# Performance work log

Measured on AMD Instinct MI355X. Metric: run time of the kernel, lower is better.

## Reference

```python
import jax, jax.numpy as jnp
import numpy as np

FORGET_BIAS = 1.0  # tf.nn.rnn_cell.LSTMCell default


def _lstm_scan(x_btE, W, b, hidden):
    """x: (B,T,E). W: (E+H, 4H), gate order i, j, f, o (TF LSTMCell)."""
    B = x_btE.shape[0]
    h0 = jnp.zeros((B, hidden), x_btE.dtype)
    c0 = jnp.zeros((B, hidden), x_btE.dtype)

    def step(carry, x_t):
        h, c = carry
        z = jnp.concatenate([x_t, h], axis=-1) @ W + b  # (B, 4H)
        i, j, f, o = jnp.split(z, 4, axis=-1)
        c_new = jax.nn.sigmoid(f + FORGET_BIAS) * c + jax.nn.sigmoid(i) * jnp.tanh(j)
        h_new = jax.nn.sigmoid(o) * jnp.tanh(c_new)
        return (h_new, c_new), h_new

    (_, _), hs = jax.lax.scan(step, (h0, c0), jnp.swapaxes(x_btE, 0, 1))
    return jnp.swapaxes(hs, 0, 1)  # (B, T, H)


def setup_inputs() -> dict:
    key = jax.random.key(0)
    ks = jax.random.split(key, 5)
    B, T, V, E, H, C = 256, 120, 50000, 256, 1024, 5
    tokens = jax.random.randint(ks[0], (B, T, 1), 0, V, dtype=jnp.int32)
    embeddings = jax.random.normal(ks[1], (V, E), jnp.float32) * 0.1
    W_lstm = jax.random.normal(ks[2], (E + H, 4 * H), jnp.float32) * (1.0 / np.sqrt(E + H))
    b_lstm = jnp.zeros((4 * H,), jnp.float32)
    U = jax.random.normal(ks[3], (H, C), jnp.float32) * (1.0 / np.sqrt(H))
    b2 = jnp.zeros((C,), jnp.float32)
    return {"tokens": tokens, "embeddings": embeddings, "W_lstm": W_lstm,
            "b_lstm": b_lstm, "U": U, "b2": b2}


def reference(tokens, embeddings, W_lstm, b_lstm, U, b2):
    B, T, F = tokens.shape  # F == n_features == 1
    E = embeddings.shape[1]
    H = U.shape[0]
    # embedding lookup + reshape to (B, T, F*E)
    x = embeddings[tokens].reshape(B, T, F * E)
    outputs = _lstm_scan(x, W_lstm, b_lstm, H)  # (B, T, H); dropout keep_prob=1 -> identity
    preds = outputs.reshape(-1, H) @ U + b2
    return preds.reshape(B, T, -1)  # (B, max_length, n_classes)
```

## Files before the change

kernel.cpp:

```cpp
#include <hip/hip_runtime.h>

typedef unsigned short u16;
typedef unsigned int u32;
typedef unsigned long long u64;
typedef int   v4i  __attribute__((ext_vector_type(4)));
typedef short v8s  __attribute__((ext_vector_type(8)));
typedef float v2f  __attribute__((ext_vector_type(2)));
typedef float v16f __attribute__((ext_vector_type(16)));

#define B_ 256
#define T_ 120
#define E_ 256
#define H_ 1024
#define K_ 1280
#define LDH 1032
#define LDX 264

#define WS_WF   0
#define WS_X    10485760
#define WS_HS   26214400
#define WS_BAR  89128960

__device__ __forceinline__ u16 f2bf(float f) {
    union { float f; u32 u; } v; v.f = f;
    u32 r = v.u + 0x7fffu + ((v.u >> 16) & 1u);
    return (u16)(r >> 16);
}
__device__ __forceinline__ float bf2f(u16 u) {
    union { u32 u; float f; } v; v.u = ((u32)u) << 16; return v.f;
}
__device__ __forceinline__ float fsig(float x) {
    float t = __builtin_amdgcn_exp2f(-1.44269504f * x);
    return __builtin_amdgcn_rcpf(1.0f + t);
}
__device__ __forceinline__ float ftanh_(float x) {
    float xc = fminf(8.0f, fmaxf(-8.0f, x));
    float t = __builtin_amdgcn_exp2f(2.88539008f * xc);
    return (t - 1.0f) * __builtin_amdgcn_rcpf(t + 1.0f);
}
__device__ __forceinline__ void gl_lds16(const void* g, void* l) {
    __builtin_amdgcn_global_load_lds(
        (const __attribute__((address_space(1))) void*)g,
        (__attribute__((address_space(3))) void*)l, 16, 0, 0);
}

__global__ void prep_fused(const float* __restrict__ W, u16* __restrict__ Wf,
                           const int* __restrict__ tokens, const float* __restrict__ emb,
                           u16* __restrict__ X, u32* __restrict__ bar) {
    __shared__ u16 tile[32 * 136];
    int bx  = blockIdx.x;
    int tid = threadIdx.x;

    if (bx < 1280) {
        if (bx == 0) {
            v4i z = {0, 0, 0, 0};
            *(v4i*)(bar + tid * 4) = z;
        }
        int cid = bx / 5, fo = bx % 5;
        int kh  = cid & 1, g = (cid >> 1) & 3, nc = cid >> 3;
        int colbase = g * 1024 + nc * 32;
        int c = tid & 31, r = tid >> 5;

#pragma unroll
        for (int fl = 0; fl < 8; ++fl) {
            int k0 = (2 * (fo * 8 + fl) + kh) * 16;
#pragma unroll
            for (int rr = 0; rr < 2; ++rr) {
                int row = r + rr * 8;
                float v = W[(size_t)(k0 + row) * 4096 + colbase + c];
                tile[c * 136 + fl * 16 + row] = f2bf(v);
            }
        }
        __syncthreads();

        int lane = tid & 63;
#pragma unroll
        for (int pass = 0; pass < 2; ++pass) {
            int fl = (tid >> 6) + pass * 4;
            v4i o = *(const v4i*)&tile[(lane & 31) * 136 + fl * 16 + ((lane >> 5) << 3)];
            *(v4i*)(Wf + (((size_t)(cid * 40 + fo * 8 + fl)) << 9) + lane * 8) = o;
        }
    } else {
        int v   = (bx - 1280) * 256 + tid;
        int e8  = v & 31;
        int row = v >> 5;
        int t = row >> 8, b = row & 255;
        int tok = tokens[b * T_ + t];
        const float* src = emb + (size_t)tok * E_ + e8 * 8;
        u16 o[8];
#pragma unroll
        for (int j = 0; j < 8; ++j) o[j] = f2bf(src[j]);
        *(v4i*)(X + (size_t)row * E_ + e8 * 8) = *(v4i*)o;
    }
}

__global__ __launch_bounds__(512, 2) void lstm_main(
    const u16* __restrict__ Wf, const u16* __restrict__ X,
    const float* __restrict__ b_lstm, u16* __restrict__ hs,
    u32* __restrict__ bar) {

    __shared__ u16  hbuf[32 * LDH];
    __shared__ u16  xbuf[32 * LDX];
    __shared__ float gates[2 * 4 * 32 * 34];
    __shared__ float bias[128];

    const int tid   = threadIdx.x;
    const int lane  = tid & 63;
    const int wv    = tid >> 6;
    const int g     = wv >> 1;
    const int khalf = wv & 1;
    const int bid   = blockIdx.x;
    const int mchunk = bid & 7;
    const int nc    = bid >> 3;
    const int m0    = mchunk << 5;

    if (tid < 128) bias[tid] = b_lstm[(tid >> 5) * H_ + (nc << 5) + (tid & 31)];

    v8s Wr[40];
    {
        const int cid = nc * 8 + g * 2 + khalf;
        const v4i* wsrc = (const v4i*)(Wf + (size_t)cid * 40 * 512);
#pragma unroll
        for (int f = 0; f < 40; ++f)
            Wr[f] = __builtin_bit_cast(v8s, wsrc[f * 64 + lane]);
    }
#pragma unroll
    for (int f = 0; f < 40; ++f) asm volatile("" : "+v"(Wr[f]));

    {
        const v4i* xs = (const v4i*)(X + (size_t)m0 * E_);
#pragma unroll
        for (int i = 0; i < 2; ++i) {
            int idx = tid + i * 512;
            int r = idx >> 5, c8 = idx & 31;
            *(v4i*)&xbuf[r * LDX + c8 * 8] = xs[r * 32 + c8];
        }
    }
    __syncthreads();

    const u16* Ax = &xbuf[(lane & 31) * LDX + ((lane >> 5) << 3)];
    const u16* Ah = &hbuf[(lane & 31) * LDH + ((lane >> 5) << 3)];

    v16f acc = {0,0,0,0,0,0,0,0,0,0,0,0,0,0,0,0};
#pragma unroll
    for (int f = 0; f < 8; ++f) {
        v8s a = *(const v8s*)(Ax + (2 * f + khalf) * 16);
        acc = __builtin_amdgcn_mfma_f32_32x32x16_bf16(a, Wr[f], acc, 0, 0, 0);
    }

    float cst[2] = {0.f, 0.f};
    const int cm  = tid >> 4;
    const int cn2 = (tid & 15) << 1;
    u32* hs32 = (u32*)hs;

    for (int t = 0; t < T_; ++t) {
        if (t > 0) {
            if (wv == 0) {
                u32* p = &bar[(mchunk * 32 + (lane & 31)) * 4];
                for (;;) {
                    u32 v = __hip_atomic_load(p, __ATOMIC_RELAXED,
                                              __HIP_MEMORY_SCOPE_AGENT);
                    if (__all(v >= (u32)t)) break;
                    __builtin_amdgcn_s_sleep(1);
                }
            }
            __syncthreads();
            {
                const u16* srcb = hs + ((size_t)(t - 1) * B_ + m0) * H_;
                int r0 = wv << 2;
#pragma unroll
                for (int half = 0; half < 2; ++half)
#pragma unroll
                    for (int i = 0; i < 4; ++i) {
                        int r = r0 + i;
                        gl_lds16(srcb + (size_t)r * H_ + half * 512 + lane * 8,
                                 &hbuf[r * LDH + half * 512]);
                    }
            }
            asm volatile("s_waitcnt vmcnt(4)\n\ts_barrier" ::: "memory");
#pragma unroll
            for (int f = 8; f < 24; ++f) {
                v8s a = *(const v8s*)(Ah + ((2 * f + khalf) * 16 - 256));
                acc = __builtin_amdgcn_mfma_f32_32x32x16_bf16(a, Wr[f], acc, 0, 0, 0);
            }
            asm volatile("s_waitcnt vmcnt(0)\n\ts_barrier" ::: "memory");
#pragma unroll
            for (int f = 24; f < 40; ++f) {
                v8s a = *(const v8s*)(Ah + ((2 * f + khalf) * 16 - 256));
                acc = __builtin_amdgcn_mfma_f32_32x32x16_bf16(a, Wr[f], acc, 0, 0, 0);
            }
        }

        {
            float* gb = &gates[((khalf << 2) + g) * 1088];
            int col = lane & 31, rq = (lane >> 5) << 2;
#pragma unroll
            for (int reg = 0; reg < 16; ++reg) {
                int row = (reg & 3) + ((reg >> 2) << 3) + rq;
                gb[row * 34 + col] = acc[reg];
            }
        }
        __syncthreads();

        if (t + 1 < T_) {
            const v4i* xs = (const v4i*)(X + ((size_t)(t + 1) * B_ + m0) * E_);
#pragma unroll
            for (int i = 0; i < 2; ++i) {
                int idx = tid + i * 512;
                int r = idx >> 5, c8 = idx & 31;
                *(v4i*)&xbuf[r * LDX + c8 * 8] = xs[r * 32 + c8];
            }
        }

        u32 hpack = 0;
        {
            v2f zz[4];
#pragma unroll
            for (int gg = 0; gg < 4; ++gg) {
                v2f a = *(const v2f*)&gates[gg * 1088 + cm * 34 + cn2];
                v2f b = *(const v2f*)&gates[(4 + gg) * 1088 + cm * 34 + cn2];
                zz[gg].x = a.x + b.x; zz[gg].y = a.y + b.y;
            }
#pragma unroll
            for (int q = 0; q < 2; ++q) {
                int n = cn2 + q;
                float ip = zz[0][q] + bias[n];
                float jp = zz[1][q] + bias[32 + n];
                float fp = zz[2][q] + bias[64 + n] + 1.0f;
                float op = zz[3][q] + bias[96 + n];
                float cc = fsig(fp) * cst[q] + fsig(ip) * ftanh_(jp);
                cst[q] = cc;
                hpack |= ((u32)f2bf(fsig(op) * ftanh_(cc))) << (16 * q);
            }
        }
        __hip_atomic_store(&hs32[((size_t)t * B_ + m0 + cm) * 512 + (nc << 4) + (tid & 15)],
                           hpack, __ATOMIC_RELAXED, __HIP_MEMORY_SCOPE_AGENT);

        if (t + 1 < T_) {
            asm volatile("s_waitcnt vmcnt(0)" ::: "memory");
            __syncthreads();
            if (tid == 0)
                __hip_atomic_store(&bar[(mchunk * 32 + nc) * 4], (u32)(t + 1),
                                   __ATOMIC_RELAXED, __HIP_MEMORY_SCOPE_AGENT);
#pragma unroll
            for (int reg = 0; reg < 16; ++reg) acc[reg] = 0.f;
#pragma unroll
            for (int f = 0; f < 8; ++f) {
                v8s a = *(const v8s*)(Ax + (2 * f + khalf) * 16);
                acc = __builtin_amdgcn_mfma_f32_32x32x16_bf16(a, Wr[f], acc, 0, 0, 0);
            }
        }
    }
}

__global__ void proj_kernel(const u16* __restrict__ hs, const float* __restrict__ U,
                            const float* __restrict__ b2, float* __restrict__ out) {
    __shared__ float Ul[H_ * 5];
    int tid = threadIdx.x;
    for (int i = tid; i < H_ * 5; i += 256) Ul[i] = U[i];
    __syncthreads();
    int wv = tid >> 6, lane = tid & 63;
#pragma unroll 1
    for (int i = 0; i < 16; ++i) {
        int row = blockIdx.x * 64 + wv * 16 + i;
        int t = row >> 8, b = row & 255;
        const v4i* hp = (const v4i*)(hs + (size_t)row * H_);
        float p[5] = {0.f, 0.f, 0.f, 0.f, 0.f};
#pragma unroll
        for (int half = 0; half < 2; ++half) {
            v4i hv = hp[lane * 2 + half];
            u16 us[8];
            *(v4i*)us = hv;
#pragma unroll
            for (int j = 0; j < 8; ++j) {
                float hf = bf2f(us[j]);
                int k = lane * 16 + half * 8 + j;
#pragma unroll
                for (int c = 0; c < 5; ++c) p[c] += hf * Ul[k * 5 + c];
            }
        }
#pragma unroll
        for (int c = 0; c < 5; ++c)
            for (int off = 32; off > 0; off >>= 1)
                p[c] += __shfl_down(p[c], off, 64);
        if (lane == 0) {
#pragma unroll
            for (int c = 0; c < 5; ++c)
                out[((size_t)b * T_ + t) * 5 + c] = p[c] + b2[c];
        }
    }
}

extern "C" void kernel_launch(void* const* d_in, const int* in_sizes, int n_in,
                              void* d_out, int out_size, void* d_ws, size_t ws_size,
                              hipStream_t stream) {
    const int*   tokens = (const int*)d_in[0];
    const float* emb    = (const float*)d_in[1];
    const float* W      = (const float*)d_in[2];
    const float* b_l    = (const float*)d_in[3];
    const float* U      = (const float*)d_in[4];
    const float* b2     = (const float*)d_in[5];
    float* out = (float*)d_out;

    char* ws = (char*)d_ws;
    u16* Wf  = (u16*)(ws + WS_WF);
    u16* X   = (u16*)(ws + WS_X);
    u16* hs  = (u16*)(ws + WS_HS);
    u32* bar = (u32*)(ws + WS_BAR);

    prep_fused<<<5120, 256, 0, stream>>>(W, Wf, tokens, emb, X, bar);
    lstm_main<<<256, 512, 0, stream>>>(Wf, X, b_l, hs, bar);
    proj_kernel<<<480, 256, 0, stream>>>(hs, U, b2, out);
}
```

Before: 581.0 us.

## Split LSTM gate GEMM into K-quarters per wave with two gate accumulators

Each wave now computes two gates over one quarter of the K dimension instead of one gate over half of K. Each LDS A-fragment read is reused for two MFMAs, which halves the LDS A traffic and gives two independent accumulator chains. The cost is more gate partial sums to store in LDS and reduce (four per gate), plus an extra accumulator's registers. The next-step x tile is also prefetched into registers at the top of the step so the global load overlaps the barrier wait.

```diff
diff --git a/kernel.cpp b/kernel.cpp
--- a/kernel.cpp
+++ b/kernel.cpp
@@ -101,14 +101,14 @@
 
     __shared__ u16  hbuf[32 * LDH];
     __shared__ u16  xbuf[32 * LDX];
-    __shared__ float gates[2 * 4 * 32 * 34];
+    __shared__ float gates[16 * 32 * 34];
     __shared__ float bias[128];
 
     const int tid   = threadIdx.x;
     const int lane  = tid & 63;
     const int wv    = tid >> 6;
-    const int g     = wv >> 1;
-    const int khalf = wv & 1;
+    const int kq    = wv & 3;
+    const int gg    = wv >> 2;
     const int bid   = blockIdx.x;
     const int mchunk = bid & 7;
     const int nc    = bid >> 3;
@@ -117,12 +117,16 @@
     if (tid < 128) bias[tid] = b_lstm[(tid >> 5) * H_ + (nc << 5) + (tid & 31)];
 
     v8s Wr[40];
-    {
-        const int cid = nc * 8 + g * 2 + khalf;
-        const v4i* wsrc = (const v4i*)(Wf + (size_t)cid * 40 * 512);
-#pragma unroll
-        for (int f = 0; f < 40; ++f)
-            Wr[f] = __builtin_bit_cast(v8s, wsrc[f * 64 + lane]);
+#pragma unroll
+    for (int j = 0; j < 20; ++j) {
+#pragma unroll
+        for (int gb = 0; gb < 2; ++gb) {
+            int s    = 4 * j + kq;
+            int gate = gg * 2 + gb;
+            int cid  = nc * 8 + gate * 2 + (s & 1);
+            const v4i* wsrc = (const v4i*)(Wf + (((size_t)(cid * 40 + (s >> 1))) << 9));
+            Wr[j * 2 + gb] = __builtin_bit_cast(v8s, wsrc[lane]);
+        }
     }
 #pragma unroll
     for (int f = 0; f < 40; ++f) asm volatile("" : "+v"(Wr[f]));
@@ -132,8 +136,7 @@
 #pragma unroll
         for (int i = 0; i < 2; ++i) {
             int idx = tid + i * 512;
-            int r = idx >> 5, c8 = idx & 31;
-            *(v4i*)&xbuf[r * LDX + c8 * 8] = xs[r * 32 + c8];
+            *(v4i*)&xbuf[(idx >> 5) * LDX + (idx & 31) * 8] = xs[idx];
         }
     }
     __syncthreads();
@@ -141,11 +144,13 @@
     const u16* Ax = &xbuf[(lane & 31) * LDX + ((lane >> 5) << 3)];
     const u16* Ah = &hbuf[(lane & 31) * LDH + ((lane >> 5) << 3)];
 
-    v16f acc = {0,0,0,0,0,0,0,0,0,0,0,0,0,0,0,0};
-#pragma unroll
-    for (int f = 0; f < 8; ++f) {
-        v8s a = *(const v8s*)(Ax + (2 * f + khalf) * 16);
-        acc = __builtin_amdgcn_mfma_f32_32x32x16_bf16(a, Wr[f], acc, 0, 0, 0);
+    v16f accA = {0,0,0,0,0,0,0,0,0,0,0,0,0,0,0,0};
+    v16f accB = {0,0,0,0,0,0,0,0,0,0,0,0,0,0,0,0};
+#pragma unroll
+    for (int j = 0; j < 4; ++j) {
+        v8s a = *(const v8s*)(Ax + (4 * j + kq) * 16);
+        accA = __builtin_amdgcn_mfma_f32_32x32x16_bf16(a, Wr[2 * j],     accA, 0, 0, 0);
+        accB = __builtin_amdgcn_mfma_f32_32x32x16_bf16(a, Wr[2 * j + 1], accB, 0, 0, 0);
     }
 
     float cst[2] = {0.f, 0.f};
@@ -154,6 +159,13 @@
     u32* hs32 = (u32*)hs;
 
     for (int t = 0; t < T_; ++t) {
+        v4i xr0, xr1;
+        if (t + 1 < T_) {
+            const v4i* xs = (const v4i*)(X + ((size_t)(t + 1) * B_ + m0) * E_);
+            xr0 = xs[tid];
+            xr1 = xs[tid + 512];
+        }
+
         if (t > 0) {
             if (wv == 0) {
                 u32* p = &bar[(mchunk * 32 + (lane & 31)) * 4];
@@ -179,47 +191,51 @@
             }
             asm volatile("s_waitcnt vmcnt(4)\n\ts_barrier" ::: "memory");
 #pragma unroll
-            for (int f = 8; f < 24; ++f) {
-                v8s a = *(const v8s*)(Ah + ((2 * f + khalf) * 16 - 256));
-                acc = __builtin_amdgcn_mfma_f32_32x32x16_bf16(a, Wr[f], acc, 0, 0, 0);
+            for (int j = 4; j < 12; ++j) {
+                v8s a = *(const v8s*)(Ah + ((4 * j + kq) * 16 - 256));
+                accA = __builtin_amdgcn_mfma_f32_32x32x16_bf16(a, Wr[2 * j],     accA, 0, 0, 0);
+                accB = __builtin_amdgcn_mfma_f32_32x32x16_bf16(a, Wr[2 * j + 1], accB, 0, 0, 0);
             }
             asm volatile("s_waitcnt vmcnt(0)\n\ts_barrier" ::: "memory");
 #pragma unroll
-            for (int f = 24; f < 40; ++f) {
-                v8s a = *(const v8s*)(Ah + ((2 * f + khalf) * 16 - 256));
-                acc = __builtin_amdgcn_mfma_f32_32x32x16_bf16(a, Wr[f], acc, 0, 0, 0);
+            for (int j = 12; j < 20; ++j) {
+                v8s a = *(const v8s*)(Ah + ((4 * j + kq) * 16 - 256));
+                accA = __builtin_amdgcn_mfma_f32_32x32x16_bf16(a, Wr[2 * j],     accA, 0, 0, 0);
+                accB = __builtin_amdgcn_mfma_f32_32x32x16_bf16(a, Wr[2 * j + 1], accB, 0, 0, 0);
             }
         }
 
         {
-            float* gb = &gates[((khalf << 2) + g) * 1088];
+            float* gbA = &gates[(kq * 4 + gg * 2 + 0) * 1088];
+            float* gbB = &gates[(kq * 4 + gg * 2 + 1) * 1088];
             int col = lane & 31, rq = (lane >> 5) << 2;
 #pragma unroll
             for (int reg = 0; reg < 16; ++reg) {
                 int row = (reg & 3) + ((reg >> 2) << 3) + rq;
-                gb[row * 34 + col] = acc[reg];
+                gbA[row * 34 + col] = accA[reg];
+                gbB[row * 34 + col] = accB[reg];
             }
         }
         __syncthreads();
 
         if (t + 1 < T_) {
-            const v4i* xs = (const v4i*)(X + ((size_t)(t + 1) * B_ + m0) * E_);
-#pragma unroll
-            for (int i = 0; i < 2; ++i) {
-                int idx = tid + i * 512;
-                int r = idx >> 5, c8 = idx & 31;
-                *(v4i*)&xbuf[r * LDX + c8 * 8] = xs[r * 32 + c8];
-            }
+            *(v4i*)&xbuf[(tid >> 5) * LDX + (tid & 31) * 8] = xr0;
+            int idx = tid + 512;
+            *(v4i*)&xbuf[(idx >> 5) * LDX + (idx & 31) * 8] = xr1;
         }
 
         u32 hpack = 0;
         {
             v2f zz[4];
 #pragma unroll
-            for (int gg = 0; gg < 4; ++gg) {
-                v2f a = *(const v2f*)&gates[gg * 1088 + cm * 34 + cn2];
-                v2f b = *(const v2f*)&gates[(4 + gg) * 1088 + cm * 34 + cn2];
-                zz[gg].x = a.x + b.x; zz[gg].y = a.y + b.y;
+            for (int g2 = 0; g2 < 4; ++g2) {
+                v2f s = {0.f, 0.f};
+#pragma unroll
+                for (int kk = 0; kk < 4; ++kk) {
+                    v2f a = *(const v2f*)&gates[(kk * 4 + g2) * 1088 + cm * 34 + cn2];
+                    s.x += a.x; s.y += a.y;
+                }
+                zz[g2] = s;
             }
 #pragma unroll
             for (int q = 0; q < 2; ++q) {
@@ -243,11 +259,12 @@
                 __hip_atomic_store(&bar[(mchunk * 32 + nc) * 4], (u32)(t + 1),
                                    __ATOMIC_RELAXED, __HIP_MEMORY_SCOPE_AGENT);
 #pragma unroll
-            for (int reg = 0; reg < 16; ++reg) acc[reg] = 0.f;
-#pragma unroll
-            for (int f = 0; f < 8; ++f) {
-                v8s a = *(const v8s*)(Ax + (2 * f + khalf) * 16);
-                acc = __builtin_amdgcn_mfma_f32_32x32x16_bf16(a, Wr[f], acc, 0, 0, 0);
+            for (int reg = 0; reg < 16; ++reg) { accA[reg] = 0.f; accB[reg] = 0.f; }
+#pragma unroll
+            for (int j = 0; j < 4; ++j) {
+                v8s a = *(const v8s*)(Ax + (4 * j + kq) * 16);
+                accA = __builtin_amdgcn_mfma_f32_32x32x16_bf16(a, Wr[2 * j],     accA, 0, 0, 0);
+                accB = __builtin_amdgcn_mfma_f32_32x32x16_bf16(a, Wr[2 * j + 1], accB, 0, 0, 0);
             }
         }
     }
```

Result: slower. 622.7 us (+7.2%).
